# Kernel optimization log

Hardware: AMD Instinct MI355X
Metric: run time of the kernel (lower is better)

## Reference

```python
import jax, jax.numpy as jnp
import numpy as np

N_NODES = 100000
N_EDGES = 3200000
NFEAT, NHID, NCLASS = 512, 256, 40


def setup_inputs() -> dict:
    key = jax.random.key(0)
    ks = jax.random.split(key, 8)
    x = jax.random.normal(ks[0], (N_NODES, NFEAT), dtype=jnp.float32)
    edge_row = jax.random.randint(ks[1], (N_EDGES,), 0, N_NODES, dtype=jnp.int32)
    edge_col = jax.random.randint(ks[2], (N_EDGES,), 0, N_NODES, dtype=jnp.int32)
    edge_val = jax.random.uniform(ks[3], (N_EDGES,), dtype=jnp.float32)
    W1 = jax.random.normal(ks[4], (NFEAT, NHID), dtype=jnp.float32) * (1.0 / np.sqrt(NFEAT))
    b1 = jnp.zeros((NHID,), dtype=jnp.float32)
    W2 = jax.random.normal(ks[5], (NHID, NCLASS), dtype=jnp.float32) * (1.0 / np.sqrt(NHID))
    b2 = jnp.zeros((NCLASS,), dtype=jnp.float32)
    return {"x": x, "edge_row": edge_row, "edge_col": edge_col, "edge_val": edge_val,
            "W1": W1, "b1": b1, "W2": W2, "b2": b2}


def _spmm(edge_row, edge_col, edge_val, dense):
    # out[i] = sum_{e: row[e]==i} val[e] * dense[col[e]]
    gathered = dense[edge_col] * edge_val[:, None]
    return jax.ops.segment_sum(gathered, edge_row, num_segments=N_NODES)


def reference(x, edge_row, edge_col, edge_val, W1, b1, W2, b2):
    # GraphConvolution 1: support = x@W1; out = adj @ support + b1; relu
    h = _spmm(edge_row, edge_col, edge_val, x @ W1) + b1
    h = jax.nn.relu(h)
    # dropout: inference mode (training=False) -> identity
    # GraphConvolution 2
    logits = _spmm(edge_row, edge_col, edge_val, h @ W2) + b2
    return jax.nn.log_softmax(logits, axis=1)
```

## Files before the change

kernel.cpp:

```cpp
#include <hip/hip_runtime.h>
#include <hip/hip_bf16.h>
#include <math.h>

#define N_NODES 100000
#define N_EDGES 3200000
#define NFEAT 512
#define NHID 256
#define NCLASS 40
#define LDP 40
#define NB1 256
#define RPB1 391
#define NBLK 256
#define CHUNK 12500
#define SCAP 13312
#define WTBLKS 512

#if __has_builtin(__builtin_amdgcn_cvt_pk_fp8_f32) && __has_builtin(__builtin_amdgcn_cvt_pk_f32_fp8)
#define SUP_FP8 1
#else
#define SUP_FP8 0
#endif

typedef short bf16x8 __attribute__((ext_vector_type(8)));
typedef float f32x4 __attribute__((ext_vector_type(4)));
typedef float f32x2 __attribute__((ext_vector_type(2)));
typedef unsigned long long u64;

__device__ __forceinline__ unsigned short f2bf(float f) {
    unsigned int u = __builtin_bit_cast(unsigned int, f);
    u += 0x7fffu + ((u >> 16) & 1u);
    return (unsigned short)(u >> 16);
}
__device__ __forceinline__ float bflo(unsigned int u) { return __builtin_bit_cast(float, u << 16); }
__device__ __forceinline__ float bfhi(unsigned int u) { return __builtin_bit_cast(float, u & 0xffff0000u); }
__device__ __forceinline__ unsigned int ecol_of(u64 ev) { return (unsigned int)(ev & 0xffffffffu); }
__device__ __forceinline__ float eval_of(u64 ev) { return __builtin_bit_cast(float, (unsigned int)(ev >> 32)); }

__global__ __launch_bounds__(256) void k_histA_wt(const int* __restrict__ erow, int* __restrict__ hist,
                                                  const float* __restrict__ W1, const float* __restrict__ W2,
                                                  unsigned short* __restrict__ W1T, unsigned short* __restrict__ W2T) {
    __shared__ int lh[NB1];
    const int t = threadIdx.x, blk = blockIdx.x;
    if (blk < NBLK) {
        lh[t] = 0;
        __syncthreads();
        const int base = blk * CHUNK;
        for (int i = t; i < CHUNK; i += 256)
            atomicAdd(&lh[erow[base + i] / RPB1], 1);
        __syncthreads();
        hist[blk * NB1 + t] = lh[t];
    } else {
        int i = (blk - NBLK) * 256 + t;
        int nn = i >> 9, k = i & 511;
        W1T[i] = f2bf(W1[k * NHID + nn]);
        if (i < 64 * NHID) {
            int n2 = i >> 8, k2 = i & 255;
            W2T[i] = (n2 < NCLASS) ? f2bf(W2[k2 * NCLASS + n2]) : (unsigned short)0;
        }
    }
}

__global__ __launch_bounds__(256) void k_scanB(const int* __restrict__ hist,
                                               int* __restrict__ offs, int* __restrict__ bucketptr) {
    __shared__ int sd[256];
    const int b = threadIdx.x;
    int run = 0;
#pragma unroll 8
    for (int blk = 0; blk < NBLK; ++blk) {
        int v = hist[blk * NB1 + b];
        offs[blk * NB1 + b] = run;
        run += v;
    }
    sd[b] = run;
    __syncthreads();
    for (int off = 1; off < 256; off <<= 1) {
        int x = (b >= off) ? sd[b - off] : 0;
        __syncthreads();
        sd[b] += x;
        __syncthreads();
    }
    bucketptr[b] = sd[b] - run;
    if (b == 255) bucketptr[NB1] = sd[255];
}

__global__ __launch_bounds__(256) void k_scatC(const int* __restrict__ erow, const int* __restrict__ ecol,
                                               const float* __restrict__ eval_,
                                               const int* __restrict__ hist,
                                               const int* __restrict__ offs, const int* __restrict__ bucketptr,
                                               u64* __restrict__ tmp) {
    __shared__ u64 srec[CHUNK];
    __shared__ unsigned char sbkt[CHUNK];
    __shared__ int lscan[NB1];
    __shared__ int lcur[NB1];
    __shared__ int lsegbase[NB1];
    __shared__ int sd[256];
    const int t = threadIdx.x, blk = blockIdx.x;
    const int base = blk * CHUNK;
    lsegbase[t] = bucketptr[t] + offs[blk * NB1 + t];
    int v = hist[blk * NB1 + t];
    sd[t] = v;
    __syncthreads();
    for (int off = 1; off < 256; off <<= 1) {
        int x = (t >= off) ? sd[t - off] : 0;
        __syncthreads();
        sd[t] += x;
        __syncthreads();
    }
    lscan[t] = sd[t] - v;
    lcur[t] = sd[t] - v;
    __syncthreads();
    for (int i = t; i < CHUNK; i += 256) {
        int r = erow[base + i];
        int c = ecol[base + i];
        unsigned int vb = __builtin_bit_cast(unsigned int, eval_[base + i]);
        int b = r / RPB1;
        int rl = r - b * RPB1;
        int pos = atomicAdd(&lcur[b], 1);
        srec[pos] = (u64)((unsigned int)c | ((unsigned int)rl << 17)) | ((u64)vb << 32);
        sbkt[pos] = (unsigned char)b;
    }
    __syncthreads();
    for (int i = t; i < CHUNK; i += 256) {
        int b = sbkt[i];
        __builtin_nontemporal_store(srec[i], &tmp[lsegbase[b] + (i - lscan[b])]);
    }
}

__global__ __launch_bounds__(512) void k_sortD(const int* __restrict__ bucketptr, const u64* __restrict__ tmp,
                                               u64* __restrict__ pedge, int* __restrict__ rowptr) {
    __shared__ u64 srec[SCAP];
    __shared__ int lcnt[512];
    __shared__ int sc[512];
    __shared__ int lcur[512];
    const int b = blockIdx.x, t = threadIdx.x;
    const int beg = bucketptr[b], end = bucketptr[b + 1];
    const int n = end - beg;
    lcnt[t] = 0;
    __syncthreads();
    for (int i = t; i < n; i += 512) {
        u64 rec = __builtin_nontemporal_load(&tmp[beg + i]);
        if (i < SCAP) srec[i] = rec;
        atomicAdd(&lcnt[(int)((rec >> 17) & 0x1ff)], 1);
    }
    __syncthreads();
    sc[t] = lcnt[t];
    __syncthreads();
    for (int off = 1; off < 512; off <<= 1) {
        int x = (t >= off) ? sc[t - off] : 0;
        __syncthreads();
        sc[t] += x;
        __syncthreads();
    }
    int excl = sc[t] - lcnt[t];
    lcur[t] = excl;
    if (t < RPB1) {
        int row = b * RPB1 + t;
        if (row < N_NODES) rowptr[row] = beg + excl;
    }
    if (b == NB1 - 1 && t == 0) rowptr[N_NODES] = N_EDGES;
    __syncthreads();
    for (int i = t; i < n; i += 512) {
        u64 rec = (i < SCAP) ? srec[i] : __builtin_nontemporal_load(&tmp[beg + i]);
        int rl = (int)((rec >> 17) & 0x1ff);
        int pos = atomicAdd(&lcur[rl], 1);
        pedge[beg + pos] = rec & 0xFFFFFFFF0001FFFFull;
    }
}

__global__ __launch_bounds__(512) void k_gemm1(const float* __restrict__ X,
                                               const unsigned short* __restrict__ W1T,
                                               unsigned char* __restrict__ support8) {
    __shared__ unsigned short As[2][128 * LDP];
    __shared__ unsigned short Bs[2][256 * LDP];
    const int t = threadIdx.x;
    const int lane = t & 63;
    const int w = t >> 6;
    const int wm = w >> 2, wn = w & 3;
    const int l15 = lane & 15, l4 = lane >> 4;
    const int bm = blockIdx.x;

    f32x4 acc[4][4];
#pragma unroll
    for (int m = 0; m < 4; ++m)
#pragma unroll
        for (int n = 0; n < 4; ++n) acc[m][n] = (f32x4){0.f, 0.f, 0.f, 0.f};

    const int arow = t >> 2, aq = t & 3;
    const long growA = (long)bm * 128 + arow;
    const bool avalid = growA < N_NODES;
    const float* xsrc = X + growA * NFEAT + aq * 8;
    const int brow = t >> 1, bhalf = t & 1;
    const unsigned short* bsrc = W1T + (long)brow * NFEAT + bhalf * 16;
    const int adoff = arow * LDP + aq * 8;
    const int bdoff = brow * LDP + bhalf * 16;

    float4 a0r, a1r;
    uint4 b0r, b1r;
    if (avalid) {
        a0r = *(const float4*)(xsrc + 0);
        a1r = *(const float4*)(xsrc + 4);
    } else {
        a0r = make_float4(0.f, 0.f, 0.f, 0.f);
        a1r = make_float4(0.f, 0.f, 0.f, 0.f);
    }
    b0r = *(const uint4*)(bsrc + 0);
    b1r = *(const uint4*)(bsrc + 8);
    {
        union { uint4 q; unsigned short us[8]; } u;
        const float* af = (const float*)&a0r;
#pragma unroll
        for (int j = 0; j < 4; ++j) u.us[j] = f2bf(af[j]);
        const float* af1 = (const float*)&a1r;
#pragma unroll
        for (int j = 0; j < 4; ++j) u.us[4 + j] = f2bf(af1[j]);
        *(uint4*)&As[0][adoff] = u.q;
        *(uint4*)&Bs[0][bdoff] = b0r;
        *(uint4*)&Bs[0][bdoff + 8] = b1r;
    }
    __syncthreads();

    for (int ki = 0; ki < 16; ++ki) {
        const int cur = ki & 1;
        if (ki < 15) {
            int kt = (ki + 1) * 32;
            if (avalid) {
                a0r = *(const float4*)(xsrc + kt);
                a1r = *(const float4*)(xsrc + kt + 4);
            }
            b0r = *(const uint4*)(bsrc + kt);
            b1r = *(const uint4*)(bsrc + kt + 8);
        }

        bf16x8 afr[4], bfr[4];
#pragma unroll
        for (int m = 0; m < 4; ++m)
            afr[m] = *(const bf16x8*)&As[cur][(wm * 64 + m * 16 + l15) * LDP + l4 * 8];
#pragma unroll
        for (int n = 0; n < 4; ++n)
            bfr[n] = *(const bf16x8*)&Bs[cur][(wn * 64 + n * 16 + l15) * LDP + l4 * 8];
#pragma unroll
        for (int m = 0; m < 4; ++m)
#pragma unroll
            for (int n = 0; n < 4; ++n)
                acc[m][n] = __builtin_amdgcn_mfma_f32_16x16x32_bf16(bfr[n], afr[m], acc[m][n], 0, 0, 0);

        if (ki < 15) {
            union { uint4 q; unsigned short us[8]; } u;
            const float* af = (const float*)&a0r;
#pragma unroll
            for (int j = 0; j < 4; ++j) u.us[j] = avalid ? f2bf(af[j]) : (unsigned short)0;
            const float* af1 = (const float*)&a1r;
#pragma unroll
            for (int j = 0; j < 4; ++j) u.us[4 + j] = avalid ? f2bf(af1[j]) : (unsigned short)0;
            *(uint4*)&As[cur ^ 1][adoff] = u.q;
            *(uint4*)&Bs[cur ^ 1][bdoff] = b0r;
            *(uint4*)&Bs[cur ^ 1][bdoff + 8] = b1r;
        }
        __syncthreads();
    }

#pragma unroll
    for (int m = 0; m < 4; ++m) {
        long row = (long)bm * 128 + wm * 64 + m * 16 + l15;
        if (row < N_NODES) {
#pragma unroll
            for (int n = 0; n < 4; ++n) {
                int colb = wn * 64 + n * 16 + l4 * 4;
#if SUP_FP8
                int wv = 0;
                wv = __builtin_amdgcn_cvt_pk_fp8_f32(acc[m][n][0], acc[m][n][1], wv, false);
                wv = __builtin_amdgcn_cvt_pk_fp8_f32(acc[m][n][2], acc[m][n][3], wv, true);
                *(unsigned int*)&support8[(size_t)row * NHID + colb] = (unsigned int)wv;
#else
                ushort4 o;
                o.x = f2bf(acc[m][n][0]);
                o.y = f2bf(acc[m][n][1]);
                o.z = f2bf(acc[m][n][2]);
                o.w = f2bf(acc[m][n][3]);
                *(ushort4*)&support8[(size_t)row * NHID * 2 + colb * 2] = o;
#endif
            }
        }
    }
}

__global__ __launch_bounds__(256) void k_spmm1(const int* __restrict__ rowptr,
                                               const u64* __restrict__ pedge,
                                               const unsigned char* __restrict__ support8,
                                               const float* __restrict__ b1,
                                               unsigned short* __restrict__ h) {
    int wrow = (blockIdx.x * 256 + threadIdx.x) >> 6;
    int lane = threadIdx.x & 63;
    if (wrow >= N_NODES) return;
    int beg = rowptr[wrow], end = rowptr[wrow + 1];
    float a0 = 0.f, a1 = 0.f, a2 = 0.f, a3 = 0.f;
    const int c4 = lane * 4;
    int e = beg;
#if SUP_FP8
    for (; e + 8 <= end; e += 8) {
        u64 ev[8];
#pragma unroll
        for (int j = 0; j < 8; ++j) ev[j] = __builtin_nontemporal_load(&pedge[e + j]);
        unsigned int g[8];
#pragma unroll
        for (int j = 0; j < 8; ++j)
            g[j] = *(const unsigned int*)&support8[(size_t)ecol_of(ev[j]) * NHID + c4];
#pragma unroll
        for (int j = 0; j < 8; ++j) {
            float v = eval_of(ev[j]);
            f32x2 lo = __builtin_amdgcn_cvt_pk_f32_fp8(g[j], false);
            f32x2 hi = __builtin_amdgcn_cvt_pk_f32_fp8(g[j], true);
            a0 = fmaf(v, lo[0], a0); a1 = fmaf(v, lo[1], a1);
            a2 = fmaf(v, hi[0], a2); a3 = fmaf(v, hi[1], a3);
        }
    }
    for (; e < end; ++e) {
        u64 ev = __builtin_nontemporal_load(&pedge[e]);
        float v = eval_of(ev);
        unsigned int g = *(const unsigned int*)&support8[(size_t)ecol_of(ev) * NHID + c4];
        f32x2 lo = __builtin_amdgcn_cvt_pk_f32_fp8(g, false);
        f32x2 hi = __builtin_amdgcn_cvt_pk_f32_fp8(g, true);
        a0 = fmaf(v, lo[0], a0); a1 = fmaf(v, lo[1], a1);
        a2 = fmaf(v, hi[0], a2); a3 = fmaf(v, hi[1], a3);
    }
#else
    for (; e + 8 <= end; e += 8) {
        u64 ev[8];
#pragma unroll
        for (int j = 0; j < 8; ++j) ev[j] = __builtin_nontemporal_load(&pedge[e + j]);
        uint2 g[8];
#pragma unroll
        for (int j = 0; j < 8; ++j)
            g[j] = *(const uint2*)&support8[((size_t)ecol_of(ev[j]) * NHID + c4) * 2];
#pragma unroll
        for (int j = 0; j < 8; ++j) {
            float v = eval_of(ev[j]);
            a0 = fmaf(v, bflo(g[j].x), a0); a1 = fmaf(v, bfhi(g[j].x), a1);
            a2 = fmaf(v, bflo(g[j].y), a2); a3 = fmaf(v, bfhi(g[j].y), a3);
        }
    }
    for (; e < end; ++e) {
        u64 ev = __builtin_nontemporal_load(&pedge[e]);
        float v = eval_of(ev);
        uint2 g = *(const uint2*)&support8[((size_t)ecol_of(ev) * NHID + c4) * 2];
        a0 = fmaf(v, bflo(g.x), a0); a1 = fmaf(v, bfhi(g.x), a1);
        a2 = fmaf(v, bflo(g.y), a2); a3 = fmaf(v, bfhi(g.y), a3);
    }
#endif
    float4 bb = *(const float4*)&b1[c4];
    a0 = fmaxf(a0 + bb.x, 0.f);
    a1 = fmaxf(a1 + bb.y, 0.f);
    a2 = fmaxf(a2 + bb.z, 0.f);
    a3 = fmaxf(a3 + bb.w, 0.f);
    ushort4 o;
    o.x = f2bf(a0); o.y = f2bf(a1); o.z = f2bf(a2); o.w = f2bf(a3);
    *(ushort4*)&h[(size_t)wrow * NHID + c4] = o;
}

__global__ __launch_bounds__(256) void k_gemm2(const unsigned short* __restrict__ H,
                                               const unsigned short* __restrict__ W2T,
                                               unsigned char* __restrict__ logits8) {
    __shared__ unsigned short As[128 * LDP];
    __shared__ unsigned short Bs[64 * LDP];
    const int t = threadIdx.x;
    const int lane = t & 63;
    const int w = t >> 6;
    const int wm = w >> 1, wn = w & 1;
    const int l15 = lane & 15, l4 = lane >> 4;
    const int bm = blockIdx.x;

    f32x4 acc[4][2];
#pragma unroll
    for (int m = 0; m < 4; ++m)
#pragma unroll
        for (int n = 0; n < 2; ++n) acc[m][n] = (f32x4){0.f, 0.f, 0.f, 0.f};

    const int srow = t >> 1, shalf = t & 1;
    const long grow = (long)bm * 128 + srow;
    const bool avalid = grow < N_NODES;
    const unsigned short* asrc = H + grow * NHID + shalf * 16;
    const int bn2 = t >> 2, bq = t & 3;
    const unsigned short* bsrc = W2T + bn2 * NHID + bq * 8;

    for (int kt = 0; kt < NHID; kt += 32) {
        uint4 a0, a1;
        if (avalid) {
            a0 = *(const uint4*)(asrc + kt);
            a1 = *(const uint4*)(asrc + kt + 8);
        } else {
            a0 = make_uint4(0, 0, 0, 0);
            a1 = make_uint4(0, 0, 0, 0);
        }
        uint4 bv = *(const uint4*)(bsrc + kt);
        *(uint4*)&As[srow * LDP + shalf * 16] = a0;
        *(uint4*)&As[srow * LDP + shalf * 16 + 8] = a1;
        *(uint4*)&Bs[bn2 * LDP + bq * 8] = bv;
        __syncthreads();

        bf16x8 afr[4], bfr[2];
#pragma unroll
        for (int m = 0; m < 4; ++m)
            afr[m] = *(const bf16x8*)&As[(wm * 64 + m * 16 + l15) * LDP + l4 * 8];
#pragma unroll
        for (int n = 0; n < 2; ++n)
            bfr[n] = *(const bf16x8*)&Bs[(wn * 32 + n * 16 + l15) * LDP + l4 * 8];
#pragma unroll
        for (int m = 0; m < 4; ++m)
#pragma unroll
            for (int n = 0; n < 2; ++n)
                acc[m][n] = __builtin_amdgcn_mfma_f32_16x16x32_bf16(bfr[n], afr[m], acc[m][n], 0, 0, 0);
        __syncthreads();
    }
#pragma unroll
    for (int m = 0; m < 4; ++m) {
        long row = (long)bm * 128 + wm * 64 + m * 16 + l15;
        if (row < N_NODES) {
#pragma unroll
            for (int n = 0; n < 2; ++n) {
                int colb = wn * 32 + n * 16 + l4 * 4;
                if (colb < NCLASS) {
#if SUP_FP8
                    int wv = 0;
                    wv = __builtin_amdgcn_cvt_pk_fp8_f32(acc[m][n][0], acc[m][n][1], wv, false);
                    wv = __builtin_amdgcn_cvt_pk_fp8_f32(acc[m][n][2], acc[m][n][3], wv, true);
                    *(unsigned int*)&logits8[(size_t)row * NCLASS + colb] = (unsigned int)wv;
#else
                    ushort4 o;
                    o.x = f2bf(acc[m][n][0]);
                    o.y = f2bf(acc[m][n][1]);
                    o.z = f2bf(acc[m][n][2]);
                    o.w = f2bf(acc[m][n][3]);
                    *(ushort4*)&logits8[((size_t)row * NCLASS + colb) * 2] = o;
#endif
                }
            }
        }
    }
}

__global__ __launch_bounds__(256) void k_spmm2(const int* __restrict__ rowptr,
                                               const u64* __restrict__ pedge,
                                               const unsigned char* __restrict__ logits8,
                                               const float* __restrict__ b2, float* __restrict__ out) {
    int wrow = (blockIdx.x * 256 + threadIdx.x) >> 6;
    int lane = threadIdx.x & 63;
    if (wrow >= N_NODES) return;
    int beg = rowptr[wrow], end = rowptr[wrow + 1];
    bool act = lane < 20;
    int cp = act ? lane * 2 : 0;
    float a0 = 0.f, a1 = 0.f;
    int e = beg;
#if SUP_FP8
    for (; e + 8 <= end; e += 8) {
        u64 ev[8];
#pragma unroll
        for (int j = 0; j < 8; ++j) ev[j] = __builtin_nontemporal_load(&pedge[e + j]);
        unsigned int g[8];
#pragma unroll
        for (int j = 0; j < 8; ++j)
            g[j] = (unsigned int)*(const unsigned short*)&logits8[(size_t)ecol_of(ev[j]) * NCLASS + cp];
#pragma unroll
        for (int j = 0; j < 8; ++j) {
            float v = eval_of(ev[j]);
            f32x2 lo = __builtin_amdgcn_cvt_pk_f32_fp8(g[j], false);
            a0 = fmaf(v, lo[0], a0);
            a1 = fmaf(v, lo[1], a1);
        }
    }
    for (; e < end; ++e) {
        u64 ev = __builtin_nontemporal_load(&pedge[e]);
        float v = eval_of(ev);
        unsigned int g = (unsigned int)*(const unsigned short*)&logits8[(size_t)ecol_of(ev) * NCLASS + cp];
        f32x2 lo = __builtin_amdgcn_cvt_pk_f32_fp8(g, false);
        a0 = fmaf(v, lo[0], a0);
        a1 = fmaf(v, lo[1], a1);
    }
#else
    for (; e + 8 <= end; e += 8) {
        u64 ev[8];
#pragma unroll
        for (int j = 0; j < 8; ++j) ev[j] = __builtin_nontemporal_load(&pedge[e + j]);
        unsigned int g[8];
#pragma unroll
        for (int j = 0; j < 8; ++j)
            g[j] = *(const unsigned int*)&logits8[((size_t)ecol_of(ev[j]) * NCLASS + cp) * 2];
#pragma unroll
        for (int j = 0; j < 8; ++j) {
            float v = eval_of(ev[j]);
            a0 = fmaf(v, bflo(g[j]), a0);
            a1 = fmaf(v, bfhi(g[j]), a1);
        }
    }
    for (; e < end; ++e) {
        u64 ev = __builtin_nontemporal_load(&pedge[e]);
        float v = eval_of(ev);
        unsigned int g = *(const unsigned int*)&logits8[((size_t)ecol_of(ev) * NCLASS + cp) * 2];
        a0 = fmaf(v, bflo(g), a0);
        a1 = fmaf(v, bfhi(g), a1);
    }
#endif
    float2 bb = *(const float2*)&b2[cp];
    a0 += bb.x;
    a1 += bb.y;
    float mv = act ? fmaxf(a0, a1) : -INFINITY;
#pragma unroll
    for (int off = 32; off; off >>= 1) mv = fmaxf(mv, __shfl_xor(mv, off, 64));
    float s = act ? (__expf(a0 - mv) + __expf(a1 - mv)) : 0.f;
#pragma unroll
    for (int off = 32; off; off >>= 1) s += __shfl_xor(s, off, 64);
    if (act) {
        float ls = __logf(s);
        float2 o;
        o.x = a0 - mv - ls;
        o.y = a1 - mv - ls;
        *(float2*)&out[(size_t)wrow * NCLASS + cp] = o;
    }
}

extern "C" void kernel_launch(void* const* d_in, const int* in_sizes, int n_in,
                              void* d_out, int out_size, void* d_ws, size_t ws_size,
                              hipStream_t stream) {
    const float* x    = (const float*)d_in[0];
    const int*   erow = (const int*)d_in[1];
    const int*   ecol = (const int*)d_in[2];
    const float* eval_ = (const float*)d_in[3];
    const float* W1   = (const float*)d_in[4];
    const float* b1   = (const float*)d_in[5];
    const float* W2   = (const float*)d_in[6];
    const float* b2   = (const float*)d_in[7];
    float* out = (float*)d_out;

    char* p = (char*)d_ws;
    auto alloc = [&](size_t b) { char* r = p; p += (b + 255) & ~(size_t)255; return r; };
    int* hist              = (int*)alloc((size_t)NBLK * NB1 * 4);
    int* offs              = (int*)alloc((size_t)NBLK * NB1 * 4);
    int* bucketptr         = (int*)alloc((size_t)(NB1 + 1) * 4);
    int* rowptr            = (int*)alloc((size_t)(N_NODES + 1) * 4);
    u64* tmp               = (u64*)alloc((size_t)N_EDGES * 8);
    u64* pedge             = (u64*)alloc((size_t)N_EDGES * 8);
    unsigned short* W1T    = (unsigned short*)alloc((size_t)NHID * NFEAT * 2);
    unsigned short* W2T    = (unsigned short*)alloc((size_t)64 * NHID * 2);
    unsigned char* support8= (unsigned char*)alloc((size_t)N_NODES * NHID * 2);
    unsigned short* h      = (unsigned short*)alloc((size_t)N_NODES * NHID * 2);
    unsigned char* logits8 = (unsigned char*)alloc((size_t)N_NODES * NCLASS * 2);

    k_histA_wt<<<NBLK + WTBLKS, 256, 0, stream>>>(erow, hist, W1, W2, W1T, W2T);
    k_scanB<<<1, 256, 0, stream>>>(hist, offs, bucketptr);
    k_scatC<<<NBLK, 256, 0, stream>>>(erow, ecol, eval_, hist, offs, bucketptr, tmp);
    k_sortD<<<NB1, 512, 0, stream>>>(bucketptr, tmp, pedge, rowptr);
    k_gemm1<<<(N_NODES + 127) / 128, 512, 0, stream>>>(x, W1T, support8);
    k_spmm1<<<(N_NODES + 3) / 4, 256, 0, stream>>>(rowptr, pedge, support8, b1, h);
    k_gemm2<<<(N_NODES + 127) / 128, 256, 0, stream>>>(h, W2T, logits8);
    k_spmm2<<<(N_NODES + 3) / 4, 256, 0, stream>>>(rowptr, pedge, logits8, b2, out);
}
```

Measured before the change: 452.8 us.

## Split spmm2 wave into 8 edge groups with 8-column lanes

Reorganizes the second SpMM kernel so each wavefront lane handles one of 8 edge groups and 8 contiguous columns, instead of 20 active lanes each handling 2 columns over all edges. This uses more lanes per wave and issues wider per-lane gathers, aiming to expose more memory-level parallelism on the random logits gathers. The partial sums are then reduced across edge groups with cross-lane shuffles, and log-softmax is reduced within 8-lane groups. It drops the previous 8-edge unrolled batching of loads, which may lower per-lane load concurrency, and it adds shuffle reduction cost.

```diff
diff --git a/kernel.cpp b/kernel.cpp
--- a/kernel.cpp
+++ b/kernel.cpp
@@ -446,74 +446,72 @@
     int lane = threadIdx.x & 63;
     if (wrow >= N_NODES) return;
     int beg = rowptr[wrow], end = rowptr[wrow + 1];
-    bool act = lane < 20;
-    int cp = act ? lane * 2 : 0;
-    float a0 = 0.f, a1 = 0.f;
-    int e = beg;
+    const int eg = lane >> 3;
+    const int cl = lane & 7;
+    const bool colact = cl < 5;
+    const int cb = colact ? cl * 8 : 0;
+    float acc[8];
+#pragma unroll
+    for (int j = 0; j < 8; ++j) acc[j] = 0.f;
 #if SUP_FP8
-    for (; e + 8 <= end; e += 8) {
-        u64 ev[8];
-#pragma unroll
-        for (int j = 0; j < 8; ++j) ev[j] = __builtin_nontemporal_load(&pedge[e + j]);
-        unsigned int g[8];
-#pragma unroll
-        for (int j = 0; j < 8; ++j)
-            g[j] = (unsigned int)*(const unsigned short*)&logits8[(size_t)ecol_of(ev[j]) * NCLASS + cp];
-#pragma unroll
-        for (int j = 0; j < 8; ++j) {
-            float v = eval_of(ev[j]);
-            f32x2 lo = __builtin_amdgcn_cvt_pk_f32_fp8(g[j], false);
-            a0 = fmaf(v, lo[0], a0);
-            a1 = fmaf(v, lo[1], a1);
-        }
-    }
-    for (; e < end; ++e) {
+    for (int e = beg + eg; e < end; e += 8) {
         u64 ev = __builtin_nontemporal_load(&pedge[e]);
         float v = eval_of(ev);
-        unsigned int g = (unsigned int)*(const unsigned short*)&logits8[(size_t)ecol_of(ev) * NCLASS + cp];
-        f32x2 lo = __builtin_amdgcn_cvt_pk_f32_fp8(g, false);
-        a0 = fmaf(v, lo[0], a0);
-        a1 = fmaf(v, lo[1], a1);
+        uint2 g = *(const uint2*)&logits8[(size_t)ecol_of(ev) * NCLASS + cb];
+        f32x2 p0 = __builtin_amdgcn_cvt_pk_f32_fp8(g.x, false);
+        f32x2 p1 = __builtin_amdgcn_cvt_pk_f32_fp8(g.x, true);
+        f32x2 p2 = __builtin_amdgcn_cvt_pk_f32_fp8(g.y, false);
+        f32x2 p3 = __builtin_amdgcn_cvt_pk_f32_fp8(g.y, true);
+        acc[0] = fmaf(v, p0[0], acc[0]); acc[1] = fmaf(v, p0[1], acc[1]);
+        acc[2] = fmaf(v, p1[0], acc[2]); acc[3] = fmaf(v, p1[1], acc[3]);
+        acc[4] = fmaf(v, p2[0], acc[4]); acc[5] = fmaf(v, p2[1], acc[5]);
+        acc[6] = fmaf(v, p3[0], acc[6]); acc[7] = fmaf(v, p3[1], acc[7]);
     }
 #else
-    for (; e + 8 <= end; e += 8) {
-        u64 ev[8];
-#pragma unroll
-        for (int j = 0; j < 8; ++j) ev[j] = __builtin_nontemporal_load(&pedge[e + j]);
-        unsigned int g[8];
-#pragma unroll
-        for (int j = 0; j < 8; ++j)
-            g[j] = *(const unsigned int*)&logits8[((size_t)ecol_of(ev[j]) * NCLASS + cp) * 2];
-#pragma unroll
-        for (int j = 0; j < 8; ++j) {
-            float v = eval_of(ev[j]);
-            a0 = fmaf(v, bflo(g[j]), a0);
-            a1 = fmaf(v, bfhi(g[j]), a1);
-        }
-    }
-    for (; e < end; ++e) {
+    for (int e = beg + eg; e < end; e += 8) {
         u64 ev = __builtin_nontemporal_load(&pedge[e]);
         float v = eval_of(ev);
-        unsigned int g = *(const unsigned int*)&logits8[((size_t)ecol_of(ev) * NCLASS + cp) * 2];
-        a0 = fmaf(v, bflo(g), a0);
-        a1 = fmaf(v, bfhi(g), a1);
+        uint4 g = *(const uint4*)&logits8[((size_t)ecol_of(ev) * NCLASS + cb) * 2];
+        acc[0] = fmaf(v, bflo(g.x), acc[0]); acc[1] = fmaf(v, bfhi(g.x), acc[1]);
+        acc[2] = fmaf(v, bflo(g.y), acc[2]); acc[3] = fmaf(v, bfhi(g.y), acc[3]);
+        acc[4] = fmaf(v, bflo(g.z), acc[4]); acc[5] = fmaf(v, bfhi(g.z), acc[5]);
+        acc[6] = fmaf(v, bflo(g.w), acc[6]); acc[7] = fmaf(v, bfhi(g.w), acc[7]);
     }
 #endif
-    float2 bb = *(const float2*)&b2[cp];
-    a0 += bb.x;
-    a1 += bb.y;
-    float mv = act ? fmaxf(a0, a1) : -INFINITY;
-#pragma unroll
-    for (int off = 32; off; off >>= 1) mv = fmaxf(mv, __shfl_xor(mv, off, 64));
-    float s = act ? (__expf(a0 - mv) + __expf(a1 - mv)) : 0.f;
-#pragma unroll
-    for (int off = 32; off; off >>= 1) s += __shfl_xor(s, off, 64);
-    if (act) {
+#pragma unroll
+    for (int off = 8; off < 64; off <<= 1)
+#pragma unroll
+        for (int j = 0; j < 8; ++j)
+            acc[j] += __shfl_xor(acc[j], off, 64);
+    if (colact) {
+        float4 bb0 = *(const float4*)&b2[cb];
+        float4 bb1 = *(const float4*)&b2[cb + 4];
+        acc[0] += bb0.x; acc[1] += bb0.y; acc[2] += bb0.z; acc[3] += bb0.w;
+        acc[4] += bb1.x; acc[5] += bb1.y; acc[6] += bb1.z; acc[7] += bb1.w;
+    }
+    float mv = -INFINITY;
+    if (colact) {
+#pragma unroll
+        for (int j = 0; j < 8; ++j) mv = fmaxf(mv, acc[j]);
+    }
+#pragma unroll
+    for (int off = 1; off < 8; off <<= 1) mv = fmaxf(mv, __shfl_xor(mv, off, 64));
+    float s = 0.f;
+    if (colact) {
+#pragma unroll
+        for (int j = 0; j < 8; ++j) s += __expf(acc[j] - mv);
+    }
+#pragma unroll
+    for (int off = 1; off < 8; off <<= 1) s += __shfl_xor(s, off, 64);
+    if (colact && eg == 0) {
         float ls = __logf(s);
-        float2 o;
-        o.x = a0 - mv - ls;
-        o.y = a1 - mv - ls;
-        *(float2*)&out[(size_t)wrow * NCLASS + cp] = o;
+        float4 o0, o1;
+        o0.x = acc[0] - mv - ls; o0.y = acc[1] - mv - ls;
+        o0.z = acc[2] - mv - ls; o0.w = acc[3] - mv - ls;
+        o1.x = acc[4] - mv - ls; o1.y = acc[5] - mv - ls;
+        o1.z = acc[6] - mv - ls; o1.w = acc[7] - mv - ls;
+        *(float4*)&out[(size_t)wrow * NCLASS + cb] = o0;
+        *(float4*)&out[(size_t)wrow * NCLASS + cb + 4] = o1;
     }
 }
 
```

New measurement: 412.8 us, median of 2. 1.1x faster.
